# Performance work log

Measured on AMD Instinct MI355X. Metric: run time of the kernel, lower is better.

The kernel has to match this reference:

```python
import jax, jax.numpy as jnp
import numpy as np

N_NODES = 500000
N_EDGES = 8000000


def gcn_conv(x, W, b, src, dst, n_nodes):
    # PyG GCNConv: add self-loops, symmetric normalization, x@W, scatter-add.
    loop = jnp.arange(n_nodes, dtype=src.dtype)
    src_a = jnp.concatenate([src, loop])  # [E+N]
    dst_a = jnp.concatenate([dst, loop])
    deg = jax.ops.segment_sum(jnp.ones_like(dst_a, dtype=x.dtype), dst_a,
                              num_segments=n_nodes)  # in-degree incl. self-loop
    dinv = jnp.where(deg > 0, jax.lax.rsqrt(deg), 0.0)
    norm = dinv[src_a] * dinv[dst_a]  # [E+N]
    xw = x @ W  # [N, out]
    msg = xw[src_a] * norm[:, None]  # [E+N, out]
    out = jax.ops.segment_sum(msg, dst_a, num_segments=n_nodes)
    return out + b


def setup_inputs() -> dict:
    key = jax.random.key(0)
    k1, k2, k3, k4, k5, k6 = jax.random.split(key, 6)
    x = jax.random.uniform(k1, (N_NODES, 1), dtype=jnp.float32)
    edge_index = jax.random.randint(k2, (2, N_EDGES), 0, N_NODES, dtype=jnp.int32)
    W1 = jax.random.normal(k3, (1, 16), dtype=jnp.float32)
    b1 = jax.random.normal(k4, (16,), dtype=jnp.float32) * 0.1
    W2 = jax.random.normal(k5, (16, 2), dtype=jnp.float32)
    b2 = jax.random.normal(k6, (2,), dtype=jnp.float32) * 0.1
    return {"x": x, "edge_index": edge_index, "W1": W1, "b1": b1,
            "W2": W2, "b2": b2}


def reference(x, edge_index, W1, b1, W2, b2):
    src, dst = edge_index[0], edge_index[1]
    h = gcn_conv(x, W1, b1, src, dst, N_NODES)
    h = jax.nn.relu(h)
    # dropout is identity in eval mode
    h = gcn_conv(h, W2, b2, src, dst, N_NODES)
    return jax.nn.log_softmax(h, axis=1)
```

## Files before the change

kernel.cpp:

```cpp
#include <hip/hip_runtime.h>
#include <math.h>


typedef unsigned int uint4v __attribute__((ext_vector_type(4)));

#define NPB 1024
#define NPB_SHIFT 10
#define NPB_MASK (NPB - 1)
#define MAXB 512
#define P1T 512
#define CHUNK 16384
#define EPT 32
#define SORT_CAP 17408
#define SPT 17
#define AGG_T 1024

__device__ __forceinline__ unsigned short f2bf(float f) {
    unsigned int x = __float_as_uint(f);
    x += 0x7fffu + ((x >> 16) & 1u);
    return (unsigned short)(x >> 16);
}
__device__ __forceinline__ float bf2f(unsigned short h) {
    return __uint_as_float((unsigned int)h << 16);
}

__global__ __launch_bounds__(P1T) void k_bucket(
    const int* __restrict__ src, const int* __restrict__ dst,
    unsigned int* __restrict__ file, int* __restrict__ ctr,
    int E, int nbucket, int cap)
{
    __shared__ unsigned int sorted[CHUNK];
    __shared__ int rk[MAXB];
    __shared__ int pre[MAXB + 1];
    __shared__ int gb[MAXB];
    __shared__ int wsum[P1T / 64];

    const int t  = threadIdx.x;
    const int e0 = blockIdx.x * CHUNK;
    const int nE = min(CHUNK, E - e0);

    for (int b = t; b < MAXB; b += P1T) rk[b] = 0;
    __syncthreads();

    const bool full = (nE == CHUNK);
    int4 dc[8];
    int  rnk[EPT];

    if (full) {
        const int4* d4 = (const int4*)(dst + e0);
#pragma unroll
        for (int k = 0; k < 8; ++k) dc[k] = d4[t + k * P1T];
#pragma unroll
        for (int k = 0; k < 8; ++k) {
            rnk[4 * k]     = atomicAdd(&rk[((unsigned)dc[k].x) >> NPB_SHIFT], 1);
            rnk[4 * k + 1] = atomicAdd(&rk[((unsigned)dc[k].y) >> NPB_SHIFT], 1);
            rnk[4 * k + 2] = atomicAdd(&rk[((unsigned)dc[k].z) >> NPB_SHIFT], 1);
            rnk[4 * k + 3] = atomicAdd(&rk[((unsigned)dc[k].w) >> NPB_SHIFT], 1);
        }
    } else {
        int k = 0;
        for (int i = t; i < nE; i += P1T, ++k)
            rnk[k] = atomicAdd(&rk[((unsigned)dst[e0 + i]) >> NPB_SHIFT], 1);
    }
    __syncthreads();

    {
        const int lane = t & 63, wv = t >> 6;
        int v = (t < nbucket) ? rk[t] : 0;
#pragma unroll
        for (int d = 1; d < 64; d <<= 1) {
            int nv = __shfl_up(v, d, 64);
            if (lane >= d) v += nv;
        }
        if (lane == 63) wsum[wv] = v;
        __syncthreads();
        if (t < P1T / 64) {
            int s = wsum[t];
#pragma unroll
            for (int d = 1; d < P1T / 64; d <<= 1) {
                int ns = __shfl_up(s, d, P1T / 64);
                if (t >= d) s += ns;
            }
            wsum[t] = s;
        }
        __syncthreads();
        pre[t + 1] = (wv ? wsum[wv - 1] : 0) + v;
        if (t == 0) pre[0] = 0;
    }
    __syncthreads();

    for (int b = t; b < nbucket; b += P1T) {
        int c = pre[b + 1] - pre[b];
        gb[b] = c ? atomicAdd(&ctr[b], c) : 0;
    }
    __syncthreads();

    if (full) {
        const int4* s4 = (const int4*)(src + e0);
#pragma unroll
        for (int k = 0; k < 8; ++k) {
            int4 s = s4[t + k * P1T];
            int4 d = dc[k];
            sorted[pre[((unsigned)d.x) >> NPB_SHIFT] + rnk[4 * k]] =
                (((unsigned)s.x) << NPB_SHIFT) | ((unsigned)d.x & NPB_MASK);
            sorted[pre[((unsigned)d.y) >> NPB_SHIFT] + rnk[4 * k + 1]] =
                (((unsigned)s.y) << NPB_SHIFT) | ((unsigned)d.y & NPB_MASK);
            sorted[pre[((unsigned)d.z) >> NPB_SHIFT] + rnk[4 * k + 2]] =
                (((unsigned)s.z) << NPB_SHIFT) | ((unsigned)d.z & NPB_MASK);
            sorted[pre[((unsigned)d.w) >> NPB_SHIFT] + rnk[4 * k + 3]] =
                (((unsigned)s.w) << NPB_SHIFT) | ((unsigned)d.w & NPB_MASK);
        }
    } else {
        int k = 0;
        for (int i = t; i < nE; i += P1T, ++k) {
            int d = dst[e0 + i];
            int b = ((unsigned)d) >> NPB_SHIFT;
            sorted[pre[b] + rnk[k]] =
                (((unsigned)src[e0 + i]) << NPB_SHIFT) | ((unsigned)d & NPB_MASK);
        }
    }
    __syncthreads();

    {
        const int wid  = t >> 6;
        const int lane = t & 63;
        const int nw   = P1T >> 6;
        for (int b = wid; b < nbucket; b += nw) {
            int s0 = pre[b], s1 = pre[b + 1];
            int base = gb[b];
            unsigned int* dp = file + (size_t)b * cap;
            for (int j = s0 + lane; j < s1; j += 64) {
                int idx = base + (j - s0);
                if (idx < cap)
                    __builtin_nontemporal_store(sorted[j], &dp[idx]);
            }
        }
    }
}

__global__ __launch_bounds__(NPB) void k_sort(
    unsigned int* __restrict__ file, const int* __restrict__ ctr,
    const float* __restrict__ x, float* __restrict__ dinv,
    unsigned short* __restrict__ u, int N, int cap)
{
    __shared__ unsigned int sorted[SORT_CAP];
    __shared__ int cnt[NPB];
    __shared__ int pre[NPB + 1];
    __shared__ int wsum[NPB / 64];

    const int t = threadIdx.x;
    const int b = blockIdx.x;
    const int nb = min(ctr[b], cap);
    unsigned int* f = file + (size_t)b * cap;

    cnt[t] = 0;
    __syncthreads();

    unsigned int ev[SPT];
    int rk_[SPT];
#pragma unroll
    for (int k = 0; k < SPT; ++k) {
        int i = t + (k << NPB_SHIFT);
        if (i < nb) ev[k] = __builtin_nontemporal_load(f + i);
    }
#pragma unroll
    for (int k = 0; k < SPT; ++k) {
        int i = t + (k << NPB_SHIFT);
        if (i < nb) rk_[k] = atomicAdd(&cnt[ev[k] & NPB_MASK], 1);
    }
    __syncthreads();

    {
        const int lane = t & 63, wv = t >> 6;
        int v = cnt[t];
#pragma unroll
        for (int d = 1; d < 64; d <<= 1) {
            int nv = __shfl_up(v, d, 64);
            if (lane >= d) v += nv;
        }
        if (lane == 63) wsum[wv] = v;
        __syncthreads();
        if (t < NPB / 64) {
            int s = wsum[t];
#pragma unroll
            for (int d = 1; d < NPB / 64; d <<= 1) {
                int ns = __shfl_up(s, d, NPB / 64);
                if (t >= d) s += ns;
            }
            wsum[t] = s;
        }
        __syncthreads();
        pre[t + 1] = (wv ? wsum[wv - 1] : 0) + v;
        if (t == 0) pre[0] = 0;
    }
    __syncthreads();

#pragma unroll
    for (int k = 0; k < SPT; ++k) {
        int i = t + (k << NPB_SHIFT);
        if (i < nb)
            sorted[pre[ev[k] & NPB_MASK] + rk_[k]] = ev[k];
    }
    __syncthreads();

    for (int i = t; i < nb; i += NPB)
        __builtin_nontemporal_store(sorted[i], &f[i]);

    const int g = b * NPB + t;
    if (g < N) {
        float dv = rsqrtf((float)(cnt[t] + 1));
        dinv[g] = dv;
        u[g] = f2bf(x[g] * dv);
    }
}

__global__ __launch_bounds__(AGG_T) void k_agg1(
    const unsigned int* __restrict__ file, const int* __restrict__ ctr,
    const unsigned short* __restrict__ u, const float* __restrict__ dinv,
    const float* __restrict__ W1, const float* __restrict__ b1,
    const float* __restrict__ W2, unsigned int* __restrict__ q,
    int N, int cap)
{
    __shared__ float acc[NPB];
    const int t = threadIdx.x;
    const int b = blockIdx.x;
    const int lane = t & 63;
    const int nb = min(ctr[b], cap);
    const unsigned int* f = file + (size_t)b * cap;

    acc[t] = 0.f;
    __syncthreads();

    const int nbr = (nb + 63) & ~63;
    for (int i = t; i < nbr; i += AGG_T) {
        bool valid = (i < nb);
        unsigned int w = valid ? __builtin_nontemporal_load(f + i) : 0u;
        int key = valid ? (int)(w & NPB_MASK) : -1;
        float val = valid ? bf2f(u[w >> NPB_SHIFT]) : 0.f;
#pragma unroll
        for (int d = 1; d < 64; d <<= 1) {
            float nv = __shfl_up(val, d, 64);
            int   nk = __shfl_up(key, d, 64);
            if (lane >= d && nk == key) val += nv;
        }
        int kd = __shfl_down(key, 1, 64);
        if (valid && (lane == 63 || kd != key))
            atomicAdd(&acc[key], val);
    }
    __syncthreads();

    const int g = b * NPB + t;
    if (g < N) {
        float dv = dinv[g];
        float s1v = (acc[t] + bf2f(u[g])) * dv;
        float c0 = 0.f, c1 = 0.f;
#pragma unroll
        for (int k = 0; k < 16; ++k) {
            float h = fmaxf(fmaf(s1v, W1[k], b1[k]), 0.f);
            c0 = fmaf(h, W2[2 * k], c0);
            c1 = fmaf(h, W2[2 * k + 1], c1);
        }
        q[g] = (unsigned int)f2bf(c0 * dv) | ((unsigned int)f2bf(c1 * dv) << 16);
    }
}

__global__ __launch_bounds__(AGG_T) void k_agg2(
    const unsigned int* __restrict__ file, const int* __restrict__ ctr,
    const unsigned int* __restrict__ q, const float* __restrict__ dinv,
    const float* __restrict__ b2, float2* __restrict__ out,
    int N, int cap)
{
    __shared__ float a0s[NPB];
    __shared__ float a1s[NPB];
    const int t = threadIdx.x;
    const int b = blockIdx.x;
    const int lane = t & 63;
    const int nb = min(ctr[b], cap);
    const unsigned int* f = file + (size_t)b * cap;

    a0s[t] = 0.f;
    a1s[t] = 0.f;
    __syncthreads();

    const int nbr = (nb + 63) & ~63;
    for (int i = t; i < nbr; i += AGG_T) {
        bool valid = (i < nb);
        unsigned int w = valid ? __builtin_nontemporal_load(f + i) : 0u;
        int key = valid ? (int)(w & NPB_MASK) : -1;
        float v0 = 0.f, v1 = 0.f;
        if (valid) {
            unsigned int gq = q[w >> NPB_SHIFT];
            v0 = bf2f((unsigned short)gq);
            v1 = bf2f((unsigned short)(gq >> 16));
        }
#pragma unroll
        for (int d = 1; d < 64; d <<= 1) {
            float n0 = __shfl_up(v0, d, 64);
            float n1 = __shfl_up(v1, d, 64);
            int   nk = __shfl_up(key, d, 64);
            if (lane >= d && nk == key) { v0 += n0; v1 += n1; }
        }
        int kd = __shfl_down(key, 1, 64);
        if (valid && (lane == 63 || kd != key)) {
            atomicAdd(&a0s[key], v0);
            atomicAdd(&a1s[key], v1);
        }
    }
    __syncthreads();

    const int g = b * NPB + t;
    if (g < N) {
        float dv = dinv[g];
        unsigned int qi = q[g];
        float o0 = (a0s[t] + bf2f((unsigned short)qi)) * dv + b2[0];
        float o1 = (a1s[t] + bf2f((unsigned short)(qi >> 16))) * dv + b2[1];
        float m = fmaxf(o0, o1);
        float l = m + logf(expf(o0 - m) + expf(o1 - m));
        out[g] = make_float2(o0 - l, o1 - l);
    }
}

#define NT 256
__global__ __launch_bounds__(NT) void fb_deg(const int* __restrict__ dst,
                                             int* __restrict__ deg, int E) {
    int e = blockIdx.x * blockDim.x + threadIdx.x;
    if (e < E) atomicAdd(&deg[dst[e]], 1);
}
__global__ __launch_bounds__(NT) void fb_node1(const float* __restrict__ x,
                                               const int* __restrict__ deg,
                                               float* __restrict__ dinv,
                                               float* __restrict__ u, int N) {
    int i = blockIdx.x * blockDim.x + threadIdx.x;
    if (i < N) {
        float dv = rsqrtf((float)(deg[i] + 1));
        dinv[i] = dv;
        u[i] = x[i] * dv;
    }
}
__global__ __launch_bounds__(NT) void fb_edge1(const int* __restrict__ src,
                                               const int* __restrict__ dst,
                                               const float* __restrict__ u,
                                               float* __restrict__ agg1, int E) {
    int e = blockIdx.x * blockDim.x + threadIdx.x;
    if (e < E) atomicAdd(&agg1[dst[e]], u[src[e]]);
}
__global__ __launch_bounds__(NT) void fb_node2(const float* __restrict__ agg1,
                                               const float* __restrict__ u,
                                               const float* __restrict__ dinv,
                                               const float* __restrict__ W1,
                                               const float* __restrict__ b1,
                                               const float* __restrict__ W2,
                                               float2* __restrict__ q, int N) {
    int i = blockIdx.x * blockDim.x + threadIdx.x;
    if (i < N) {
        float dv = dinv[i];
        float s1 = (agg1[i] + u[i]) * dv;
        float c0 = 0.f, c1 = 0.f;
#pragma unroll
        for (int k = 0; k < 16; ++k) {
            float h = fmaxf(fmaf(s1, W1[k], b1[k]), 0.f);
            c0 = fmaf(h, W2[2 * k], c0);
            c1 = fmaf(h, W2[2 * k + 1], c1);
        }
        q[i] = make_float2(c0 * dv, c1 * dv);
    }
}
__global__ __launch_bounds__(NT) void fb_edge2(const int* __restrict__ src,
                                               const int* __restrict__ dst,
                                               const float2* __restrict__ q,
                                               float* __restrict__ agg2, int E) {
    int e = blockIdx.x * blockDim.x + threadIdx.x;
    if (e < E) {
        float2 qq = q[src[e]];
        atomicAdd(&agg2[2 * dst[e]], qq.x);
        atomicAdd(&agg2[2 * dst[e] + 1], qq.y);
    }
}
__global__ __launch_bounds__(NT) void fb_node3(const float* __restrict__ agg2,
                                               const float2* __restrict__ q,
                                               const float* __restrict__ dinv,
                                               const float* __restrict__ b2,
                                               float2* __restrict__ out, int N) {
    int i = blockIdx.x * blockDim.x + threadIdx.x;
    if (i < N) {
        float dv = dinv[i];
        float2 qi = q[i];
        float o0 = (agg2[2 * i] + qi.x) * dv + b2[0];
        float o1 = (agg2[2 * i + 1] + qi.y) * dv + b2[1];
        float m = fmaxf(o0, o1);
        float l = m + logf(expf(o0 - m) + expf(o1 - m));
        out[i] = make_float2(o0 - l, o1 - l);
    }
}

extern "C" void kernel_launch(void* const* d_in, const int* in_sizes, int n_in,
                              void* d_out, int out_size, void* d_ws, size_t ws_size,
                              hipStream_t stream) {
    const float* x  = (const float*)d_in[0];
    const int* ei   = (const int*)d_in[1];
    const float* W1 = (const float*)d_in[2];
    const float* b1 = (const float*)d_in[3];
    const float* W2 = (const float*)d_in[4];
    const float* b2 = (const float*)d_in[5];

    const int N = in_sizes[0];
    const int E = in_sizes[1] / 2;
    const int* src = ei;
    const int* dst = ei + E;

    const int nbucket = (N + NPB - 1) / NPB;
    const int cap = ((E / nbucket + 1024) + 63) & ~63;

    auto align_up = [](size_t v) { return (v + 255) & ~(size_t)255; };
    size_t off_ctr   = 0;
    size_t off_file  = align_up((size_t)MAXB * sizeof(int));
    size_t off_dinv  = align_up(off_file + (size_t)nbucket * SORT_CAP * sizeof(unsigned int));
    size_t off_u     = align_up(off_dinv + (size_t)N * sizeof(float));
    size_t off_q     = align_up(off_u + (size_t)N * sizeof(unsigned short));
    size_t needed    = off_q + (size_t)N * sizeof(unsigned int);

    char* ws = (char*)d_ws;

    if (nbucket <= MAXB && cap <= SORT_CAP && needed <= ws_size) {
        int*            ctr   = (int*)(ws + off_ctr);
        unsigned int*   file  = (unsigned int*)(ws + off_file);
        float*          dinv  = (float*)(ws + off_dinv);
        unsigned short* u     = (unsigned short*)(ws + off_u);
        unsigned int*   q     = (unsigned int*)(ws + off_q);

        (void)hipMemsetAsync(ctr, 0, (size_t)MAXB * sizeof(int), stream);

        const int p1Blocks = (E + CHUNK - 1) / CHUNK;
        k_bucket<<<p1Blocks, P1T, 0, stream>>>(src, dst, file, ctr, E, nbucket, SORT_CAP);
        k_sort  <<<nbucket, NPB, 0, stream>>>(file, ctr, x, dinv, u, N, SORT_CAP);
        k_agg1  <<<nbucket, AGG_T, 0, stream>>>(file, ctr, u, dinv, W1, b1, W2, q, N, SORT_CAP);
        k_agg2  <<<nbucket, AGG_T, 0, stream>>>(file, ctr, q, dinv, b2, (float2*)d_out, N, SORT_CAP);
    } else {
        int*    deg  = (int*)   (ws);
        float*  agg1 = (float*) (ws + (size_t)4 * N);
        float*  agg2 = (float*) (ws + (size_t)8 * N);
        float*  dinv = (float*) (ws + (size_t)16 * N);
        float*  u    = (float*) (ws + (size_t)20 * N);
        float2* q    = (float2*)(ws + (size_t)24 * N);
        (void)hipMemsetAsync(ws, 0, (size_t)16 * N, stream);
        const int nodeBlocks = (N + NT - 1) / NT;
        const int edgeBlocks = (E + NT - 1) / NT;
        fb_deg  <<<edgeBlocks, NT, 0, stream>>>(dst, deg, E);
        fb_node1<<<nodeBlocks, NT, 0, stream>>>(x, deg, dinv, u, N);
        fb_edge1<<<edgeBlocks, NT, 0, stream>>>(src, dst, u, agg1, E);
        fb_node2<<<nodeBlocks, NT, 0, stream>>>(agg1, u, dinv, W1, b1, W2, q, N);
        fb_edge2<<<edgeBlocks, NT, 0, stream>>>(src, dst, q, agg2, E);
        fb_node3<<<nodeBlocks, NT, 0, stream>>>(agg2, q, dinv, b2, (float2*)d_out, N);
    }
}
```

Before: 241.8 us.

## Fuse sort and both aggregation passes into one cooperative kernel with grid syncs

```diff
diff --git a/kernel.cpp b/kernel.cpp
--- a/kernel.cpp
+++ b/kernel.cpp
@@ -1,8 +1,9 @@
 #include <hip/hip_runtime.h>
+#include <hip/hip_cooperative_groups.h>
 #include <math.h>
 
-
-typedef unsigned int uint4v __attribute__((ext_vector_type(4)));
+namespace cg = cooperative_groups;
+
 
 #define NPB 1024
 #define NPB_SHIFT 10
@@ -13,7 +14,6 @@
 #define EPT 32
 #define SORT_CAP 17408
 #define SPT 17
-#define AGG_T 1024
 
 __device__ __forceinline__ unsigned short f2bf(float f) {
     unsigned int x = __float_as_uint(f);
@@ -138,6 +138,125 @@
     }
 }
 
+__global__ __launch_bounds__(NPB, 8) void k_fused(
+    const unsigned int* __restrict__ file, const int* __restrict__ ctr,
+    const float* __restrict__ x, unsigned short* __restrict__ u,
+    unsigned int* __restrict__ q, const float* __restrict__ W1,
+    const float* __restrict__ b1, const float* __restrict__ W2,
+    const float* __restrict__ b2, float2* __restrict__ out,
+    int N, int cap)
+{
+    __shared__ unsigned int sorted[SORT_CAP];
+    __shared__ int cnt[NPB];
+    __shared__ int pre[NPB + 1];
+    __shared__ int wsum[NPB / 64];
+
+    const int t = threadIdx.x;
+    const int b = blockIdx.x;
+    const int nb = min(ctr[b], cap);
+    const unsigned int* f = file + (size_t)b * cap;
+    const int g = b * NPB + t;
+
+    cg::grid_group grid = cg::this_grid();
+
+    cnt[t] = 0;
+    __syncthreads();
+
+    unsigned int ev[SPT];
+    int rk_[SPT];
+#pragma unroll
+    for (int k = 0; k < SPT; ++k) {
+        int i = t + (k << NPB_SHIFT);
+        if (i < nb) ev[k] = __builtin_nontemporal_load(f + i);
+    }
+#pragma unroll
+    for (int k = 0; k < SPT; ++k) {
+        int i = t + (k << NPB_SHIFT);
+        if (i < nb) rk_[k] = atomicAdd(&cnt[ev[k] & NPB_MASK], 1);
+    }
+    __syncthreads();
+
+    {
+        const int lane = t & 63, wv = t >> 6;
+        int v = cnt[t];
+#pragma unroll
+        for (int d = 1; d < 64; d <<= 1) {
+            int nv = __shfl_up(v, d, 64);
+            if (lane >= d) v += nv;
+        }
+        if (lane == 63) wsum[wv] = v;
+        __syncthreads();
+        if (t < NPB / 64) {
+            int s = wsum[t];
+#pragma unroll
+            for (int d = 1; d < NPB / 64; d <<= 1) {
+                int ns = __shfl_up(s, d, NPB / 64);
+                if (t >= d) s += ns;
+            }
+            wsum[t] = s;
+        }
+        __syncthreads();
+        pre[t + 1] = (wv ? wsum[wv - 1] : 0) + v;
+        if (t == 0) pre[0] = 0;
+    }
+    __syncthreads();
+
+#pragma unroll
+    for (int k = 0; k < SPT; ++k) {
+        int i = t + (k << NPB_SHIFT);
+        if (i < nb)
+            sorted[pre[ev[k] & NPB_MASK] + rk_[k]] = ev[k];
+    }
+
+    float dv = 0.f, uself = 0.f;
+    if (g < N) {
+        dv = rsqrtf((float)(cnt[t] + 1));
+        uself = x[g] * dv;
+        u[g] = f2bf(uself);
+    }
+    grid.sync();
+
+    float q0self = 0.f, q1self = 0.f;
+    {
+        int e0 = pre[t], e1 = pre[t + 1];
+        float acc = 0.f;
+        for (int j = e0; j < e1; ++j)
+            acc += bf2f(u[sorted[j] >> NPB_SHIFT]);
+        if (g < N) {
+            float s1v = (acc + uself) * dv;
+            float c0 = 0.f, c1 = 0.f;
+#pragma unroll
+            for (int k = 0; k < 16; ++k) {
+                float h = fmaxf(fmaf(s1v, W1[k], b1[k]), 0.f);
+                c0 = fmaf(h, W2[2 * k], c0);
+                c1 = fmaf(h, W2[2 * k + 1], c1);
+            }
+            q0self = c0 * dv;
+            q1self = c1 * dv;
+            q[g] = (unsigned int)f2bf(q0self) |
+                   ((unsigned int)f2bf(q1self) << 16);
+        }
+    }
+    grid.sync();
+
+    {
+        int e0 = pre[t], e1 = pre[t + 1];
+        float a0 = 0.f, a1 = 0.f;
+        for (int j = e0; j < e1; ++j) {
+            unsigned int gq = q[sorted[j] >> NPB_SHIFT];
+            a0 += bf2f((unsigned short)gq);
+            a1 += bf2f((unsigned short)(gq >> 16));
+        }
+        if (g < N) {
+            float o0 = (a0 + q0self) * dv + b2[0];
+            float o1 = (a1 + q1self) * dv + b2[1];
+            float m = fmaxf(o0, o1);
+            float l = m + logf(expf(o0 - m) + expf(o1 - m));
+            out[g] = make_float2(o0 - l, o1 - l);
+        }
+    }
+}
+
 __global__ __launch_bounds__(NPB) void k_sort(
     unsigned int* __restrict__ file, const int* __restrict__ ctr,
     const float* __restrict__ x, float* __restrict__ dinv,
@@ -208,189 +327,78 @@
 
     const int g = b * NPB + t;
     if (g < N) {
-        float dv = rsqrtf((float)(cnt[t] + 1));
-        dinv[g] = dv;
-        u[g] = f2bf(x[g] * dv);
-    }
-}
-
-__global__ __launch_bounds__(AGG_T) void k_agg1(
+        float dvv = rsqrtf((float)(cnt[t] + 1));
+        dinv[g] = dvv;
+        u[g] = f2bf(x[g] * dvv);
+    }
+}
+
+__global__ __launch_bounds__(256) void k_agg1(
     const unsigned int* __restrict__ file, const int* __restrict__ ctr,
     const unsigned short* __restrict__ u, const float* __restrict__ dinv,
     const float* __restrict__ W1, const float* __restrict__ b1,
     const float* __restrict__ W2, unsigned int* __restrict__ q,
     int N, int cap)
 {
-    __shared__ float acc[NPB];
-    const int t = threadIdx.x;
-    const int b = blockIdx.x;
-    const int lane = t & 63;
-    const int nb = min(ctr[b], cap);
+    int g = blockIdx.x * 256 + threadIdx.x;
+    if (g >= N) return;
+    int b = g >> NPB_SHIFT, loc = g & NPB_MASK;
     const unsigned int* f = file + (size_t)b * cap;
-
-    acc[t] = 0.f;
-    __syncthreads();
-
-    const int nbr = (nb + 63) & ~63;
-    for (int i = t; i < nbr; i += AGG_T) {
-        bool valid = (i < nb);
-        unsigned int w = valid ? __builtin_nontemporal_load(f + i) : 0u;
-        int key = valid ? (int)(w & NPB_MASK) : -1;
-        float val = valid ? bf2f(u[w >> NPB_SHIFT]) : 0.f;
-#pragma unroll
-        for (int d = 1; d < 64; d <<= 1) {
-            float nv = __shfl_up(val, d, 64);
-            int   nk = __shfl_up(key, d, 64);
-            if (lane >= d && nk == key) val += nv;
-        }
-        int kd = __shfl_down(key, 1, 64);
-        if (valid && (lane == 63 || kd != key))
-            atomicAdd(&acc[key], val);
-    }
-    __syncthreads();
-
-    const int g = b * NPB + t;
-    if (g < N) {
-        float dv = dinv[g];
-        float s1v = (acc[t] + bf2f(u[g])) * dv;
-        float c0 = 0.f, c1 = 0.f;
-#pragma unroll
-        for (int k = 0; k < 16; ++k) {
-            float h = fmaxf(fmaf(s1v, W1[k], b1[k]), 0.f);
-            c0 = fmaf(h, W2[2 * k], c0);
-            c1 = fmaf(h, W2[2 * k + 1], c1);
-        }
-        q[g] = (unsigned int)f2bf(c0 * dv) | ((unsigned int)f2bf(c1 * dv) << 16);
-    }
-}
-
-__global__ __launch_bounds__(AGG_T) void k_agg2(
+    int nb = min(ctr[b], cap);
+    float acc = 0.f;
+    int lo = 0, hi = nb;
+    while (lo < hi) {
+        int mid = (lo + hi) >> 1;
+        if ((int)(f[mid] & NPB_MASK) < loc) lo = mid + 1; else hi = mid;
+    }
+    for (int j = lo; j < nb; ++j) {
+        unsigned int w = f[j];
+        if ((int)(w & NPB_MASK) != loc) break;
+        acc += bf2f(u[w >> NPB_SHIFT]);
+    }
+    float dvv = dinv[g];
+    float s1v = (acc + bf2f(u[g])) * dvv;
+    float c0 = 0.f, c1 = 0.f;
+#pragma unroll
+    for (int k = 0; k < 16; ++k) {
+        float h = fmaxf(fmaf(s1v, W1[k], b1[k]), 0.f);
+        c0 = fmaf(h, W2[2 * k], c0);
+        c1 = fmaf(h, W2[2 * k + 1], c1);
+    }
+    q[g] = (unsigned int)f2bf(c0 * dvv) | ((unsigned int)f2bf(c1 * dvv) << 16);
+}
+
+__global__ __launch_bounds__(256) void k_agg2(
     const unsigned int* __restrict__ file, const int* __restrict__ ctr,
     const unsigned int* __restrict__ q, const float* __restrict__ dinv,
     const float* __restrict__ b2, float2* __restrict__ out,
     int N, int cap)
 {
-    __shared__ float a0s[NPB];
-    __shared__ float a1s[NPB];
-    const int t = threadIdx.x;
-    const int b = blockIdx.x;
-    const int lane = t & 63;
-    const int nb = min(ctr[b], cap);
+    int g = blockIdx.x * 256 + threadIdx.x;
+    if (g >= N) return;
+    int b = g >> NPB_SHIFT, loc = g & NPB_MASK;
     const unsigned int* f = file + (size_t)b * cap;
-
-    a0s[t] = 0.f;
-    a1s[t] = 0.f;
-    __syncthreads();
-
-    const int nbr = (nb + 63) & ~63;
-    for (int i = t; i < nbr; i += AGG_T) {
-        bool valid = (i < nb);
-        unsigned int w = valid ? __builtin_nontemporal_load(f + i) : 0u;
-        int key = valid ? (int)(w & NPB_MASK) : -1;
-        float v0 = 0.f, v1 = 0.f;
-        if (valid) {
-            unsigned int gq = q[w >> NPB_SHIFT];
-            v0 = bf2f((unsigned short)gq);
-            v1 = bf2f((unsigned short)(gq >> 16));
-        }
-#pragma unroll
-        for (int d = 1; d < 64; d <<= 1) {
-            float n0 = __shfl_up(v0, d, 64);
-            float n1 = __shfl_up(v1, d, 64);
-            int   nk = __shfl_up(key, d, 64);
-            if (lane >= d && nk == key) { v0 += n0; v1 += n1; }
-        }
-        int kd = __shfl_down(key, 1, 64);
-        if (valid && (lane == 63 || kd != key)) {
-            atomicAdd(&a0s[key], v0);
-            atomicAdd(&a1s[key], v1);
-        }
-    }
-    __syncthreads();
-
-    const int g = b * NPB + t;
-    if (g < N) {
-        float dv = dinv[g];
-        unsigned int qi = q[g];
-        float o0 = (a0s[t] + bf2f((unsigned short)qi)) * dv + b2[0];
-        float o1 = (a1s[t] + bf2f((unsigned short)(qi >> 16))) * dv + b2[1];
-        float m = fmaxf(o0, o1);
-        float l = m + logf(expf(o0 - m) + expf(o1 - m));
-        out[g] = make_float2(o0 - l, o1 - l);
-    }
-}
-
-#define NT 256
-__global__ __launch_bounds__(NT) void fb_deg(const int* __restrict__ dst,
-                                             int* __restrict__ deg, int E) {
-    int e = blockIdx.x * blockDim.x + threadIdx.x;
-    if (e < E) atomicAdd(&deg[dst[e]], 1);
-}
-__global__ __launch_bounds__(NT) void fb_node1(const float* __restrict__ x,
-                                               const int* __restrict__ deg,
-                                               float* __restrict__ dinv,
-                                               float* __restrict__ u, int N) {
-    int i = blockIdx.x * blockDim.x + threadIdx.x;
-    if (i < N) {
-        float dv = rsqrtf((float)(deg[i] + 1));
-        dinv[i] = dv;
-        u[i] = x[i] * dv;
-    }
-}
-__global__ __launch_bounds__(NT) void fb_edge1(const int* __restrict__ src,
-                                               const int* __restrict__ dst,
-                                               const float* __restrict__ u,
-                                               float* __restrict__ agg1, int E) {
-    int e = blockIdx.x * blockDim.x + threadIdx.x;
-    if (e < E) atomicAdd(&agg1[dst[e]], u[src[e]]);
-}
-__global__ __launch_bounds__(NT) void fb_node2(const float* __restrict__ agg1,
-                                               const float* __restrict__ u,
-                                               const float* __restrict__ dinv,
-                                               const float* __restrict__ W1,
-                                               const float* __restrict__ b1,
-                                               const float* __restrict__ W2,
-                                               float2* __restrict__ q, int N) {
-    int i = blockIdx.x * blockDim.x + threadIdx.x;
-    if (i < N) {
-        float dv = dinv[i];
-        float s1 = (agg1[i] + u[i]) * dv;
-        float c0 = 0.f, c1 = 0.f;
-#pragma unroll
-        for (int k = 0; k < 16; ++k) {
-            float h = fmaxf(fmaf(s1, W1[k], b1[k]), 0.f);
-            c0 = fmaf(h, W2[2 * k], c0);
-            c1 = fmaf(h, W2[2 * k + 1], c1);
-        }
-        q[i] = make_float2(c0 * dv, c1 * dv);
-    }
-}
-__global__ __launch_bounds__(NT) void fb_edge2(const int* __restrict__ src,
-                                               const int* __restrict__ dst,
-                                               const float2* __restrict__ q,
-                                               float* __restrict__ agg2, int E) {
-    int e = blockIdx.x * blockDim.x + threadIdx.x;
-    if (e < E) {
-        float2 qq = q[src[e]];
-        atomicAdd(&agg2[2 * dst[e]], qq.x);
-        atomicAdd(&agg2[2 * dst[e] + 1], qq.y);
-    }
-}
-__global__ __launch_bounds__(NT) void fb_node3(const float* __restrict__ agg2,
-                                               const float2* __restrict__ q,
-                                               const float* __restrict__ dinv,
-                                               const float* __restrict__ b2,
-                                               float2* __restrict__ out, int N) {
-    int i = blockIdx.x * blockDim.x + threadIdx.x;
-    if (i < N) {
-        float dv = dinv[i];
-        float2 qi = q[i];
-        float o0 = (agg2[2 * i] + qi.x) * dv + b2[0];
-        float o1 = (agg2[2 * i + 1] + qi.y) * dv + b2[1];
-        float m = fmaxf(o0, o1);
-        float l = m + logf(expf(o0 - m) + expf(o1 - m));
-        out[i] = make_float2(o0 - l, o1 - l);
-    }
+    int nb = min(ctr[b], cap);
+    float a0 = 0.f, a1 = 0.f;
+    int lo = 0, hi = nb;
+    while (lo < hi) {
+        int mid = (lo + hi) >> 1;
+        if ((int)(f[mid] & NPB_MASK) < loc) lo = mid + 1; else hi = mid;
+    }
+    for (int j = lo; j < nb; ++j) {
+        unsigned int w = f[j];
+        if ((int)(w & NPB_MASK) != loc) break;
+        unsigned int gq = q[w >> NPB_SHIFT];
+        a0 += bf2f((unsigned short)gq);
+        a1 += bf2f((unsigned short)(gq >> 16));
+    }
+    float dvv = dinv[g];
+    unsigned int qi = q[g];
+    float o0 = (a0 + bf2f((unsigned short)qi)) * dvv + b2[0];
+    float o1 = (a1 + bf2f((unsigned short)(qi >> 16))) * dvv + b2[1];
+    float m = fmaxf(o0, o1);
+    float l = m + logf(expf(o0 - m) + expf(o1 - m));
+    out[g] = make_float2(o0 - l, o1 - l);
 }
 
 extern "C" void kernel_launch(void* const* d_in, const int* in_sizes, int n_in,
@@ -421,35 +429,39 @@
 
     char* ws = (char*)d_ws;
 
+    int*            ctr   = (int*)(ws + off_ctr);
+    unsigned int*   file  = (unsigned int*)(ws + off_file);
+    float*          dinv  = (float*)(ws + off_dinv);
+    unsigned short* u     = (unsigned short*)(ws + off_u);
+    unsigned int*   q     = (unsigned int*)(ws + off_q);
+    float2*         outp  = (float2*)d_out;
+
     if (nbucket <= MAXB && cap <= SORT_CAP && needed <= ws_size) {
-        int*            ctr   = (int*)(ws + off_ctr);
-        unsigned int*   file  = (unsigned int*)(ws + off_file);
-        float*          dinv  = (float*)(ws + off_dinv);
-        unsigned short* u     = (unsigned short*)(ws + off_u);
-        unsigned int*   q     = (unsigned int*)(ws + off_q);
-
         (void)hipMemsetAsync(ctr, 0, (size_t)MAXB * sizeof(int), stream);
 
         const int p1Blocks = (E + CHUNK - 1) / CHUNK;
         k_bucket<<<p1Blocks, P1T, 0, stream>>>(src, dst, file, ctr, E, nbucket, SORT_CAP);
-        k_sort  <<<nbucket, NPB, 0, stream>>>(file, ctr, x, dinv, u, N, SORT_CAP);
-        k_agg1  <<<nbucket, AGG_T, 0, stream>>>(file, ctr, u, dinv, W1, b1, W2, q, N, SORT_CAP);
-        k_agg2  <<<nbucket, AGG_T, 0, stream>>>(file, ctr, q, dinv, b2, (float2*)d_out, N, SORT_CAP);
+
+        int capv = SORT_CAP, Nv = N;
+        void* args[] = {(void*)&file, (void*)&ctr, (void*)&x, (void*)&u,
+                        (void*)&q, (void*)&W1, (void*)&b1, (void*)&W2,
+                        (void*)&b2, (void*)&outp, (void*)&Nv, (void*)&capv};
+        hipError_t err = hipLaunchCooperativeKernel(
+            (const void*)k_fused, dim3(nbucket), dim3(NPB), args, 0, stream);
+
+        if (err != hipSuccess) {
+            const int nodBlocks = (N + 255) / 256;
+            k_sort<<<nbucket, NPB, 0, stream>>>(file, ctr, x, dinv, u, N, SORT_CAP);
+            k_agg1<<<nodBlocks, 256, 0, stream>>>(file, ctr, u, dinv, W1, b1, W2, q, N, SORT_CAP);
+            k_agg2<<<nodBlocks, 256, 0, stream>>>(file, ctr, q, dinv, b2, outp, N, SORT_CAP);
+        }
     } else {
-        int*    deg  = (int*)   (ws);
-        float*  agg1 = (float*) (ws + (size_t)4 * N);
-        float*  agg2 = (float*) (ws + (size_t)8 * N);
-        float*  dinv = (float*) (ws + (size_t)16 * N);
-        float*  u    = (float*) (ws + (size_t)20 * N);
-        float2* q    = (float2*)(ws + (size_t)24 * N);
-        (void)hipMemsetAsync(ws, 0, (size_t)16 * N, stream);
-        const int nodeBlocks = (N + NT - 1) / NT;
-        const int edgeBlocks = (E + NT - 1) / NT;
-        fb_deg  <<<edgeBlocks, NT, 0, stream>>>(dst, deg, E);
-        fb_node1<<<nodeBlocks, NT, 0, stream>>>(x, deg, dinv, u, N);
-        fb_edge1<<<edgeBlocks, NT, 0, stream>>>(src, dst, u, agg1, E);
-        fb_node2<<<nodeBlocks, NT, 0, stream>>>(agg1, u, dinv, W1, b1, W2, q, N);
-        fb_edge2<<<edgeBlocks, NT, 0, stream>>>(src, dst, q, agg2, E);
-        fb_node3<<<nodeBlocks, NT, 0, stream>>>(agg2, q, dinv, b2, (float2*)d_out, N);
-    }
-}
+        (void)hipMemsetAsync(ctr, 0, (size_t)MAXB * sizeof(int), stream);
+        const int p1Blocks = (E + CHUNK - 1) / CHUNK;
+        const int nodBlocks = (N + 255) / 256;
+        k_bucket<<<p1Blocks, P1T, 0, stream>>>(src, dst, file, ctr, E, nbucket, SORT_CAP);
+        k_sort<<<nbucket, NPB, 0, stream>>>(file, ctr, x, dinv, u, N, SORT_CAP);
+        k_agg1<<<nodBlocks, 256, 0, stream>>>(file, ctr, u, dinv, W1, b1, W2, q, N, SORT_CAP);
+        k_agg2<<<nodBlocks, 256, 0, stream>>>(file, ctr, q, dinv, b2, outp, N, SORT_CAP);
+    }
+}
```

After: 330.4 us. 1.37x slower.
